# Performance work log

Hardware: AMD Instinct MI355X
Metric: run time of the kernel (lower is better)

The kernel has to match this reference:

```python
import jax, jax.numpy as jnp
import numpy as np

IN_DIM, OUT_DIM = 256, 64
ALPHA = 0.2  # leaky relu negative slope
NEG_INF = -1e30


def setup_inputs() -> dict:
    key = jax.random.key(0)
    k1, k2, k3, k4 = jax.random.split(key, 4)
    B, N = 8, 2048
    h = jax.random.normal(k1, (B, N, IN_DIM), dtype=jnp.float32)
    adj = jax.random.randint(k2, (B, N, N), 0, 2, dtype=jnp.int32)
    # ensure no fully-isolated node (avoids softmax over all -inf)
    idx = jnp.arange(N)
    adj = adj.at[:, idx, idx].set(1)
    # params: fc.weight [out,in] -> store transposed [in,out]; attn_fc.weight [1, 2*out] -> [2*out]
    W = jax.random.normal(k3, (IN_DIM, OUT_DIM), dtype=jnp.float32) / np.sqrt(IN_DIM)
    a = jax.random.normal(k4, (2 * OUT_DIM,), dtype=jnp.float32) / np.sqrt(2 * OUT_DIM)
    return {"h": h, "adj": adj, "W": W, "a": a}


def reference(h, adj, W, a):
    # Wh: [B,N,D]
    Wh = jnp.einsum("bni,io->bno", h, W)
    D = Wh.shape[-1]
    # concat-based additive attention decomposed: e[b,i,j] = lrelu(a1.Wh_i + a2.Wh_j)
    a1, a2 = a[:D], a[D:]
    s1 = Wh @ a1  # [B,N] contribution of row node i
    s2 = Wh @ a2  # [B,N] contribution of col node j
    e = jax.nn.leaky_relu(s1[:, :, None] + s2[:, None, :], negative_slope=ALPHA)  # [B,N,N]
    e = jnp.where(adj == 0, NEG_INF, e)
    attn = jax.nn.softmax(e, axis=-1)
    # dropout is identity in eval mode
    return jnp.einsum("bij,bjd->bid", attn, Wh)
```

## Files before the change

### kernel.cpp

```cpp
#include <hip/hip_runtime.h>
#include <math.h>

#define NB 8
#define NN 2048
#define IN_DIM 256
#define OUT_DIM 64
#define ALPHA 0.2f
#define JSPLIT 4

typedef __attribute__((ext_vector_type(8))) short bf16x8;
typedef __attribute__((ext_vector_type(4))) float f32x4;

__device__ __forceinline__ unsigned short f2bf(float x) {
    union { float f; unsigned u; } v; v.f = x;
    unsigned r = v.u + 0x7FFF + ((v.u >> 16) & 1);
    return (unsigned short)(r >> 16);
}

#define WT_STRIDE 264
__global__ __launch_bounds__(256) void wh_kernel(const float* __restrict__ h,
                                                 const float* __restrict__ W,
                                                 const float* __restrict__ a,
                                                 unsigned short* __restrict__ Whbt,
                                                 float* __restrict__ s1,
                                                 float* __restrict__ s2) {
    __shared__ unsigned short Wt[OUT_DIM * WT_STRIDE];
    const int t = threadIdx.x;

    #pragma unroll 8
    for (int rep = 0; rep < 64; ++rep) {
        const int id = rep * 256 + t;
        const int k = id >> 6, n = id & 63;
        Wt[n * WT_STRIDE + k] = f2bf(W[id]);
    }
    __syncthreads();

    const int lane = t & 63, wv = t >> 6;
    const int m = lane & 15, quad = lane >> 4;
    const long gr0 = (long)(blockIdx.x * 4 + wv) * 16;

    f32x4 acc[4];
    #pragma unroll
    for (int nt = 0; nt < 4; ++nt) acc[nt] = (f32x4){0.f, 0.f, 0.f, 0.f};

    #pragma unroll
    for (int ks = 0; ks < 8; ++ks) {
        const int k0 = ks * 32;
        const float* hp = h + (gr0 + m) * IN_DIM + k0 + quad * 8;
        const float4 ha = *(const float4*)hp;
        const float4 hb = *(const float4*)(hp + 4);
        bf16x8 af;
        af[0] = (short)f2bf(ha.x); af[1] = (short)f2bf(ha.y);
        af[2] = (short)f2bf(ha.z); af[3] = (short)f2bf(ha.w);
        af[4] = (short)f2bf(hb.x); af[5] = (short)f2bf(hb.y);
        af[6] = (short)f2bf(hb.z); af[7] = (short)f2bf(hb.w);
        #pragma unroll
        for (int nt = 0; nt < 4; ++nt) {
            const bf16x8 bf_ = *(const bf16x8*)(const void*)
                &Wt[(nt * 16 + m) * WT_STRIDE + k0 + quad * 8];
            acc[nt] = __builtin_amdgcn_mfma_f32_16x16x32_bf16(af, bf_, acc[nt], 0, 0, 0);
        }
    }

    const int b  = (int)(gr0 >> 11);
    const int ib = (int)(gr0 & 2047);

    #pragma unroll
    for (int nt = 0; nt < 4; ++nt) {
        ushort4 w4;
        w4.x = f2bf(acc[nt][0]); w4.y = f2bf(acc[nt][1]);
        w4.z = f2bf(acc[nt][2]); w4.w = f2bf(acc[nt][3]);
        *(ushort4*)&Whbt[((long)(b * OUT_DIM + nt * 16 + m) << 11) + ib + quad * 4] = w4;
    }

    float a1v[4], a2v[4];
    #pragma unroll
    for (int nt = 0; nt < 4; ++nt) {
        a1v[nt] = a[nt * 16 + m];
        a2v[nt] = a[OUT_DIM + nt * 16 + m];
    }
    #pragma unroll
    for (int reg = 0; reg < 4; ++reg) {
        float p1 = 0.f, p2 = 0.f;
        #pragma unroll
        for (int nt = 0; nt < 4; ++nt) {
            p1 += acc[nt][reg] * a1v[nt];
            p2 += acc[nt][reg] * a2v[nt];
        }
        #pragma unroll
        for (int off = 1; off < 16; off <<= 1) {
            p1 += __shfl_xor(p1, off, 64);
            p2 += __shfl_xor(p2, off, 64);
        }
        if (m == 0) {
            s1[gr0 + quad * 4 + reg] = p1;
            s2[gr0 + quad * 4 + reg] = p2;
        }
    }
}

#define PSTR 40
__global__ __launch_bounds__(256) void attn_kernel(const int* __restrict__ adj,
                                                   const unsigned short* __restrict__ Whbt,
                                                   const float* __restrict__ s1,
                                                   const float* __restrict__ s2,
                                                   float* __restrict__ part,
                                                   float* __restrict__ lpart) {
    __shared__ unsigned short p_all[4][16 * PSTR];

    const int t = threadIdx.x, lane = t & 63, wv = t >> 6;
    unsigned short* p_lds = &p_all[wv][0];

    const int bid = blockIdx.x;
    const int js  = bid & (JSPLIT - 1);
    const int itg = (bid >> 2) & 31;
    const int b   = bid >> 7;
    const int i0  = itg * 64 + wv * 16;
    const int jlo = js * (NN / JSPLIT);

    const int rhalf = lane >> 5, jj = lane & 31;
    const int m = lane & 15, quad = lane >> 4;

    float s1r[8];
    #pragma unroll
    for (int k = 0; k < 8; ++k) s1r[k] = s1[b * NN + i0 + rhalf + 2 * k];

    f32x4 acc[4];
    #pragma unroll
    for (int nt = 0; nt < 4; ++nt) acc[nt] = (f32x4){0.f, 0.f, 0.f, 0.f};
    float lacc[8] = {0.f, 0.f, 0.f, 0.f, 0.f, 0.f, 0.f, 0.f};

    const int* adjp = adj + (long)b * NN * NN + (long)(i0 + rhalf) * NN + jlo + jj;
    const unsigned short* wbase = Whbt + ((long)(b * OUT_DIM) << 11) + jlo;
    const float* s2p = s2 + b * NN + jlo + jj;

    int av[8];
    #pragma unroll
    for (int k = 0; k < 8; ++k)
        av[k] = __builtin_nontemporal_load(adjp + (long)(2 * k) * NN);

    for (int ks = 0; ks < 16; ++ks) {
        const int j0 = ks * 32;

        bf16x8 bfr[4];
        #pragma unroll
        for (int nt = 0; nt < 4; ++nt)
            bfr[nt] = *(const bf16x8*)(const void*)
                &wbase[((long)(nt * 16 + m) << 11) + j0 + quad * 8];

        const float s2v = s2p[j0];
        #pragma unroll
        for (int k = 0; k < 8; ++k) {
            float e = s1r[k] + s2v;
            e = e > 0.f ? e : ALPHA * e;
            const float p = (av[k] != 0) ? __expf(e) : 0.f;
            lacc[k] += p;
            p_lds[(rhalf + 2 * k) * PSTR + jj] = f2bf(p);
        }

        const int jn = (ks < 15) ? j0 + 32 : j0;
        #pragma unroll
        for (int k = 0; k < 8; ++k)
            av[k] = __builtin_nontemporal_load(adjp + (long)(2 * k) * NN + jn);

        asm volatile("s_waitcnt lgkmcnt(0)" ::: "memory");

        const bf16x8 af = *(const bf16x8*)(const void*)&p_lds[m * PSTR + quad * 8];
        #pragma unroll
        for (int nt = 0; nt < 4; ++nt)
            acc[nt] = __builtin_amdgcn_mfma_f32_16x16x32_bf16(af, bfr[nt], acc[nt], 0, 0, 0);
    }

    #pragma unroll
    for (int k = 0; k < 8; ++k) {
        float s = lacc[k];
        #pragma unroll
        for (int off = 1; off < 32; off <<= 1) s += __shfl_xor(s, off, 64);
        if (jj == 0)
            lpart[js * (NB * NN) + b * NN + i0 + rhalf + 2 * k] = s;
    }

    float* pp = part + (long)js * ((long)NB * NN * OUT_DIM)
                     + ((long)(b * NN + i0) << 6);
    #pragma unroll
    for (int nt = 0; nt < 4; ++nt)
        #pragma unroll
        for (int reg = 0; reg < 4; ++reg)
            pp[(quad * 4 + reg) * OUT_DIM + nt * 16 + m] = acc[nt][reg];
}

__global__ __launch_bounds__(256) void finalize_kernel(const float* __restrict__ part,
                                                       const float* __restrict__ lpart,
                                                       float* __restrict__ out) {
    const int idx = blockIdx.x * 256 + threadIdx.x;
    const int row = idx >> 4;
    float l = 0.f;
    #pragma unroll
    for (int s = 0; s < JSPLIT; ++s) l += lpart[s * (NB * NN) + row];
    float4 v = make_float4(0.f, 0.f, 0.f, 0.f);
    const float4* p4 = (const float4*)part;
    #pragma unroll
    for (int s = 0; s < JSPLIT; ++s) {
        const float4 p = p4[(long)s * ((long)NB * NN * OUT_DIM / 4) + idx];
        v.x += p.x; v.y += p.y; v.z += p.z; v.w += p.w;
    }
    const float inv = 1.f / l;
    v.x *= inv; v.y *= inv; v.z *= inv; v.w *= inv;
    ((float4*)out)[idx] = v;
}

extern "C" void kernel_launch(void* const* d_in, const int* in_sizes, int n_in,
                              void* d_out, int out_size, void* d_ws, size_t ws_size,
                              hipStream_t stream) {
    const float* h   = (const float*)d_in[0];
    const int*   adj = (const int*)d_in[1];
    const float* W   = (const float*)d_in[2];
    const float* a   = (const float*)d_in[3];
    float* out = (float*)d_out;

    float* s1    = (float*)d_ws;
    float* s2    = s1 + NB * NN;
    float* lpart = s2 + NB * NN;
    float* part  = lpart + JSPLIT * NB * NN;
    unsigned short* Whbt = (unsigned short*)(part + (long)JSPLIT * NB * NN * OUT_DIM);

    wh_kernel<<<NB * NN / 64, 256, 0, stream>>>(h, W, a, Whbt, s1, s2);
    attn_kernel<<<NB * (NN / 64) * JSPLIT, 256, 0, stream>>>(adj, Whbt, s1, s2, part, lpart);
    finalize_kernel<<<NB * NN * OUT_DIM / 4 / 256, 256, 0, stream>>>(part, lpart, out);
}
```

Measured before the change: 231.5 us.

## Compute attention probabilities directly in MFMA A-operand layout, drop LDS staging

Each lane now loads the adjacency and s2 values that correspond to its own MFMA A-fragment elements (row m, 8 consecutive columns) as vector loads. It computes exp probabilities in registers and feeds them to the MFMA without a round-trip through shared memory and its wait. The row-sum now uses the bf16-rounded probabilities and needs a cheaper cross-lane reduction. JSPLIT goes from 4 to 8 and the loop is fully unrolled, which doubles the partial buffers and the finalize traffic. Adjacency reads are strided across 16 rows per wave, so coalescing changes.

```diff
diff --git a/kernel.cpp b/kernel.cpp
--- a/kernel.cpp
+++ b/kernel.cpp
@@ -6,15 +6,20 @@
 #define IN_DIM 256
 #define OUT_DIM 64
 #define ALPHA 0.2f
-#define JSPLIT 4
+#define JSPLIT 8
 
 typedef __attribute__((ext_vector_type(8))) short bf16x8;
 typedef __attribute__((ext_vector_type(4))) float f32x4;
+typedef __attribute__((ext_vector_type(4))) int   i32x4;
 
 __device__ __forceinline__ unsigned short f2bf(float x) {
     union { float f; unsigned u; } v; v.f = x;
     unsigned r = v.u + 0x7FFF + ((v.u >> 16) & 1);
     return (unsigned short)(r >> 16);
+}
+__device__ __forceinline__ float bf2f(unsigned short b) {
+    union { unsigned u; float f; } v; v.u = ((unsigned)b) << 16;
+    return v.f;
 }
 
 #define WT_STRIDE 264
@@ -99,86 +104,86 @@
     }
 }
 
-#define PSTR 40
+__device__ __forceinline__ float pcalc(int av, float s2e, float s1v) {
+    float e = s1v + s2e;
+    e = e > 0.f ? e : ALPHA * e;
+    const float p = __expf(e);
+    return av != 0 ? p : 0.f;
+}
+
 __global__ __launch_bounds__(256) void attn_kernel(const int* __restrict__ adj,
                                                    const unsigned short* __restrict__ Whbt,
                                                    const float* __restrict__ s1,
                                                    const float* __restrict__ s2,
                                                    float* __restrict__ part,
                                                    float* __restrict__ lpart) {
-    __shared__ unsigned short p_all[4][16 * PSTR];
-
     const int t = threadIdx.x, lane = t & 63, wv = t >> 6;
-    unsigned short* p_lds = &p_all[wv][0];
-
     const int bid = blockIdx.x;
     const int js  = bid & (JSPLIT - 1);
-    const int itg = (bid >> 2) & 31;
-    const int b   = bid >> 7;
+    const int itg = (bid >> 3) & 31;
+    const int b   = bid >> 8;
     const int i0  = itg * 64 + wv * 16;
     const int jlo = js * (NN / JSPLIT);
 
-    const int rhalf = lane >> 5, jj = lane & 31;
     const int m = lane & 15, quad = lane >> 4;
 
-    float s1r[8];
-    #pragma unroll
-    for (int k = 0; k < 8; ++k) s1r[k] = s1[b * NN + i0 + rhalf + 2 * k];
+    const int*   adjp = adj + (long)b * NN * NN + (long)(i0 + m) * NN + jlo + quad * 8;
+    const float* s2p  = s2 + b * NN + jlo + quad * 8;
+    const unsigned short* wbase = Whbt + ((long)(b * OUT_DIM) << 11) + jlo + quad * 8;
+    const float s1v = s1[b * NN + i0 + m];
 
     f32x4 acc[4];
     #pragma unroll
     for (int nt = 0; nt < 4; ++nt) acc[nt] = (f32x4){0.f, 0.f, 0.f, 0.f};
-    float lacc[8] = {0.f, 0.f, 0.f, 0.f, 0.f, 0.f, 0.f, 0.f};
-
-    const int* adjp = adj + (long)b * NN * NN + (long)(i0 + rhalf) * NN + jlo + jj;
-    const unsigned short* wbase = Whbt + ((long)(b * OUT_DIM) << 11) + jlo;
-    const float* s2p = s2 + b * NN + jlo + jj;
-
-    int av[8];
-    #pragma unroll
-    for (int k = 0; k < 8; ++k)
-        av[k] = __builtin_nontemporal_load(adjp + (long)(2 * k) * NN);
-
-    for (int ks = 0; ks < 16; ++ks) {
+    float lsum = 0.f;
+
+    i32x4  av0 = __builtin_nontemporal_load((const i32x4*)adjp);
+    i32x4  av1 = __builtin_nontemporal_load((const i32x4*)(adjp + 4));
+    float4 sv0 = *(const float4*)s2p;
+    float4 sv1 = *(const float4*)(s2p + 4);
+
+    #pragma unroll
+    for (int ks = 0; ks < NN / JSPLIT / 32; ++ks) {
         const int j0 = ks * 32;
 
         bf16x8 bfr[4];
         #pragma unroll
         for (int nt = 0; nt < 4; ++nt)
             bfr[nt] = *(const bf16x8*)(const void*)
-                &wbase[((long)(nt * 16 + m) << 11) + j0 + quad * 8];
-
-        const float s2v = s2p[j0];
-        #pragma unroll
-        for (int k = 0; k < 8; ++k) {
-            float e = s1r[k] + s2v;
-            e = e > 0.f ? e : ALPHA * e;
-            const float p = (av[k] != 0) ? __expf(e) : 0.f;
-            lacc[k] += p;
-            p_lds[(rhalf + 2 * k) * PSTR + jj] = f2bf(p);
-        }
-
-        const int jn = (ks < 15) ? j0 + 32 : j0;
-        #pragma unroll
-        for (int k = 0; k < 8; ++k)
-            av[k] = __builtin_nontemporal_load(adjp + (long)(2 * k) * NN + jn);
-
-        asm volatile("s_waitcnt lgkmcnt(0)" ::: "memory");
-
-        const bf16x8 af = *(const bf16x8*)(const void*)&p_lds[m * PSTR + quad * 8];
+                &wbase[(((long)(nt * 16 + m)) << 11) + j0];
+
+        const i32x4  ca0 = av0, ca1 = av1;
+        const float4 cs0 = sv0, cs1 = sv1;
+        if (ks < NN / JSPLIT / 32 - 1) {
+            av0 = __builtin_nontemporal_load((const i32x4*)(adjp + j0 + 32));
+            av1 = __builtin_nontemporal_load((const i32x4*)(adjp + j0 + 36));
+            sv0 = *(const float4*)(s2p + j0 + 32);
+            sv1 = *(const float4*)(s2p + j0 + 36);
+        }
+
+        float pv[8];
+        pv[0] = pcalc(ca0.x, cs0.x, s1v); pv[1] = pcalc(ca0.y, cs0.y, s1v);
+        pv[2] = pcalc(ca0.z, cs0.z, s1v); pv[3] = pcalc(ca0.w, cs0.w, s1v);
+        pv[4] = pcalc(ca1.x, cs1.x, s1v); pv[5] = pcalc(ca1.y, cs1.y, s1v);
+        pv[6] = pcalc(ca1.z, cs1.z, s1v); pv[7] = pcalc(ca1.w, cs1.w, s1v);
+
+        bf16x8 af;
+        #pragma unroll
+        for (int e = 0; e < 8; ++e) {
+            const unsigned short bb = f2bf(pv[e]);
+            af[e] = (short)bb;
+            lsum += bf2f(bb);
+        }
+
         #pragma unroll
         for (int nt = 0; nt < 4; ++nt)
             acc[nt] = __builtin_amdgcn_mfma_f32_16x16x32_bf16(af, bfr[nt], acc[nt], 0, 0, 0);
     }
 
-    #pragma unroll
-    for (int k = 0; k < 8; ++k) {
-        float s = lacc[k];
-        #pragma unroll
-        for (int off = 1; off < 32; off <<= 1) s += __shfl_xor(s, off, 64);
-        if (jj == 0)
-            lpart[js * (NB * NN) + b * NN + i0 + rhalf + 2 * k] = s;
-    }
+    lsum += __shfl_xor(lsum, 16, 64);
+    lsum += __shfl_xor(lsum, 32, 64);
+    if (quad == 0)
+        lpart[js * (NB * NN) + b * NN + i0 + m] = lsum;
 
     float* pp = part + (long)js * ((long)NB * NN * OUT_DIM)
                      + ((long)(b * NN + i0) << 6);
@@ -222,7 +227,8 @@
     float* s2    = s1 + NB * NN;
     float* lpart = s2 + NB * NN;
     float* part  = lpart + JSPLIT * NB * NN;
-    unsigned short* Whbt = (unsigned short*)(part + (long)JSPLIT * NB * NN * OUT_DIM);
+    unsigned short* Whbt =
+        (unsigned short*)(part + (long)JSPLIT * NB * NN * OUT_DIM);
 
     wh_kernel<<<NB * NN / 64, 256, 0, stream>>>(h, W, a, Whbt, s1, s2);
     attn_kernel<<<NB * (NN / 64) * JSPLIT, 256, 0, stream>>>(adj, Whbt, s1, s2, part, lpart);
```

Result: slower. 244.1 us (+5.5%).
